# Optimization experiments

Measured on AMD Instinct MI355X. Metric: run time of the kernel, lower is better.

The kernel has to match this reference:

```python
import jax, jax.numpy as jnp
import numpy as np

NEG_SLOPE = 0.01  # torch nn.LeakyReLU default; module's alpha arg is unused in forward


def setup_inputs() -> dict:
    key = jax.random.key(0)
    k1, k2, k3, k4 = jax.random.split(key, 4)
    N, IN, OUT = 16384, 256, 128
    x = jax.random.normal(k1, (N, IN), dtype=jnp.float32)
    W_tran = jax.random.normal(k2, (OUT, IN), dtype=jnp.float32) / np.sqrt(IN)
    a1 = jax.random.normal(k3, (OUT,), dtype=jnp.float32) / np.sqrt(OUT)
    a2 = jax.random.normal(k4, (OUT,), dtype=jnp.float32) / np.sqrt(OUT)
    return {"x": x, "W_tran": W_tran, "a1": a1, "a2": a2}


def reference(x, W_tran, a1, a2):
    # h = tran(x): [N, out]
    h = x @ W_tran.T
    # att1(h) -> [N], att2(h) -> [N]
    s1 = h @ a1
    s2 = h @ a2
    # e[i, j] = leakyrelu(s2[i] + s1[j])  (unsqueeze(0) broadcasts att1 over rows)
    e = jax.nn.leaky_relu(s2[:, None] + s1[None, :], negative_slope=NEG_SLOPE)  # [N, N]
    return e @ h  # [N, out]
```

## Files before the change

### kernel.cpp

```cpp
#include <hip/hip_runtime.h>
#include <hip/hip_bf16.h>
#include <stdint.h>

#define NR 16384
#define KI 256
#define MO 128
#define ALPHA 0.01f
#define CH 32
#define NCH (NR / CH)
#define RB 4
#define JT 256
#define NJ (NR / JT)

typedef unsigned long long u64;
typedef __attribute__((ext_vector_type(8))) short bf16x8;
typedef __attribute__((ext_vector_type(4))) float f32x4;

static __device__ __forceinline__ unsigned xf(float f) {
    unsigned u = __float_as_uint(f);
    return u ^ (((unsigned)((int)u >> 31)) | 0x80000000u);
}

static __device__ __forceinline__ ushort2 cvt2(float a, float b) {
    __hip_bfloat162 r = __float22bfloat162_rn(make_float2(a, b));
    return *reinterpret_cast<ushort2*>(&r);
}

static __device__ __forceinline__ unsigned f2b(float f) {
    unsigned x = __float_as_uint(f);
    return (x + 0x7fffu + ((x >> 16) & 1u)) >> 16;
}
static __device__ __forceinline__ float b2f(unsigned u) {
    return __uint_as_float(u << 16);
}
static __device__ __forceinline__ unsigned pk(float hv, float sv) {
    return f2b(hv) | (f2b(sv) << 16);
}

__global__ __launch_bounds__(256) void k_gemm_fused(const float* __restrict__ x,
                                                    const float* __restrict__ w,
                                                    const float* __restrict__ a1,
                                                    const float* __restrict__ a2,
                                                    ushort* __restrict__ hb,
                                                    float* __restrict__ s1,
                                                    float* __restrict__ s2,
                                                    unsigned* __restrict__ keys,
                                                    int* __restrict__ rank) {
    __shared__ ushort Abf[64][40];
    __shared__ ushort Bbf[128][40];
    const int t = threadIdx.x;
    const int lane = t & 63;
    const int wv = t >> 6;
    const int rowBase = blockIdx.x * 64;
    const int xr = t >> 2, xc = (t & 3) << 3;
    const int wr = t >> 1, wc = (t & 1) << 4;
    const int fr = lane & 15;
    const int fk = (lane >> 4) << 3;

    f32x4 acc[8] = {};

    float4 xv0 = *(const float4*)&x[(size_t)(rowBase + xr) * KI + xc];
    float4 xv1 = *(const float4*)&x[(size_t)(rowBase + xr) * KI + xc + 4];
    float4 wv0 = *(const float4*)&w[(size_t)wr * KI + wc];
    float4 wv1 = *(const float4*)&w[(size_t)wr * KI + wc + 4];
    float4 wv2 = *(const float4*)&w[(size_t)wr * KI + wc + 8];
    float4 wv3 = *(const float4*)&w[(size_t)wr * KI + wc + 12];

    for (int ks = 0; ks < KI / 32; ++ks) {
        __syncthreads();
        {
            union { ushort2 u2[4]; bf16x8 v; } ap;
            ap.u2[0] = cvt2(xv0.x, xv0.y); ap.u2[1] = cvt2(xv0.z, xv0.w);
            ap.u2[2] = cvt2(xv1.x, xv1.y); ap.u2[3] = cvt2(xv1.z, xv1.w);
            *(bf16x8*)&Abf[xr][xc] = ap.v;
            union { ushort2 u2[4]; bf16x8 v; } bp0, bp1;
            bp0.u2[0] = cvt2(wv0.x, wv0.y); bp0.u2[1] = cvt2(wv0.z, wv0.w);
            bp0.u2[2] = cvt2(wv1.x, wv1.y); bp0.u2[3] = cvt2(wv1.z, wv1.w);
            bp1.u2[0] = cvt2(wv2.x, wv2.y); bp1.u2[1] = cvt2(wv2.z, wv2.w);
            bp1.u2[2] = cvt2(wv3.x, wv3.y); bp1.u2[3] = cvt2(wv3.z, wv3.w);
            *(bf16x8*)&Bbf[wr][wc] = bp0.v;
            *(bf16x8*)&Bbf[wr][wc + 8] = bp1.v;
        }
        __syncthreads();
        if (ks + 1 < KI / 32) {
            int k0 = (ks + 1) * 32;
            xv0 = *(const float4*)&x[(size_t)(rowBase + xr) * KI + k0 + xc];
            xv1 = *(const float4*)&x[(size_t)(rowBase + xr) * KI + k0 + xc + 4];
            wv0 = *(const float4*)&w[(size_t)wr * KI + k0 + wc];
            wv1 = *(const float4*)&w[(size_t)wr * KI + k0 + wc + 4];
            wv2 = *(const float4*)&w[(size_t)wr * KI + k0 + wc + 8];
            wv3 = *(const float4*)&w[(size_t)wr * KI + k0 + wc + 12];
        }
        bf16x8 af = *(const bf16x8*)&Abf[wv * 16 + fr][fk];
#pragma unroll
        for (int n = 0; n < 8; ++n) {
            bf16x8 bfr = *(const bf16x8*)&Bbf[n * 16 + fr][fk];
            acc[n] = __builtin_amdgcn_mfma_f32_16x16x32_bf16(af, bfr, acc[n], 0, 0, 0);
        }
    }

    const int rq = lane >> 4;
#pragma unroll
    for (int n = 0; n < 8; ++n)
#pragma unroll
        for (int r = 0; r < 4; ++r)
            hb[(size_t)(rowBase + wv * 16 + rq * 4 + r) * MO + n * 16 + fr] = (ushort)f2b(acc[n][r]);

    float a1v[8], a2v[8];
#pragma unroll
    for (int n = 0; n < 8; ++n) { a1v[n] = a1[n * 16 + fr]; a2v[n] = a2[n * 16 + fr]; }
#pragma unroll
    for (int r = 0; r < 4; ++r) {
        float p1 = 0.f, p2 = 0.f;
#pragma unroll
        for (int n = 0; n < 8; ++n) {
            p1 = fmaf(acc[n][r], a1v[n], p1);
            p2 = fmaf(acc[n][r], a2v[n], p2);
        }
#pragma unroll
        for (int off = 8; off; off >>= 1) {
            p1 += __shfl_xor(p1, off, 64);
            p2 += __shfl_xor(p2, off, 64);
        }
        if (fr == 0) {
            int row = rowBase + wv * 16 + rq * 4 + r;
            s1[row] = p1;
            s2[row] = p2;
            keys[row] = (xf(p1) & 0xFFFFC000u) | (unsigned)row;
            rank[row] = 0;
        }
    }
}

__global__ __launch_bounds__(256) void k_rank(const unsigned* __restrict__ keys,
                                              int* __restrict__ rank) {
    __shared__ unsigned sk[JT];
    const int t = threadIdx.x;
    const int ibase = blockIdx.x * (256 * RB);
    const int jbase = blockIdx.y * JT;
    sk[t] = keys[jbase + t];
    unsigned ki[RB];
#pragma unroll
    for (int k = 0; k < RB; ++k) ki[k] = keys[ibase + k * 256 + t];
    int cnt[RB] = {};
    __syncthreads();
#pragma unroll 4
    for (int jj = 0; jj < JT; ++jj) {
        unsigned kj = sk[jj];
#pragma unroll
        for (int k = 0; k < RB; ++k)
            cnt[k] += (kj < ki[k]) ? 1 : 0;
    }
#pragma unroll
    for (int k = 0; k < RB; ++k)
        atomicAdd(&rank[ibase + k * 256 + t], cnt[k]);
}

__global__ __launch_bounds__(256) void k_scatter(const float* __restrict__ s1,
                                                 const int* __restrict__ rank,
                                                 float* __restrict__ s1s,
                                                 int* __restrict__ perm) {
    int i = blockIdx.x * 256 + threadIdx.x;
    int r = rank[i];
    s1s[r] = s1[i];
    perm[r] = i;
}

__global__ __launch_bounds__(256) void k_chunk(const ushort* __restrict__ hb,
                                               const int* __restrict__ perm,
                                               const float* __restrict__ s1s,
                                               const float* __restrict__ s2,
                                               unsigned* __restrict__ SHS,
                                               int* __restrict__ kidx) {
    __shared__ int pi[CH];
    __shared__ float ss[CH];
    __shared__ float rH[128], rS[128];
    const int t = threadIdx.x, c = t & 127, g = t >> 7, q = blockIdx.x;
    if (t < CH) { pi[t] = perm[q * CH + t]; ss[t] = s1s[q * CH + t]; }
    __syncthreads();
    float v[16];
#pragma unroll
    for (int m = 0; m < 16; ++m)
        v[m] = b2f(hb[(size_t)pi[g * 16 + m] * MO + c]);
    if (g == 1) {
        float runH = 0.f, runS = 0.f;
#pragma unroll
        for (int m = 15; m >= 0; --m) {
            runH += v[m];
            runS = fmaf(ss[16 + m], v[m], runS);
            SHS[(size_t)(q * CH + 16 + m) * MO + c] = pk(runH, runS);
        }
        rH[c] = runH; rS[c] = runS;
    } else if (t < CH) {
        int i = q * CH + t;
        unsigned qtv = xf(-s2[i]) & 0xFFFFC000u;
        int lo = 0, hi = NR;
        while (lo < hi) {
            int mid = (lo + hi) >> 1;
            if ((xf(s1s[mid]) & 0xFFFFC000u) < qtv) lo = mid + 1; else hi = mid;
        }
        kidx[i] = lo;
    }
    __syncthreads();
    if (g == 0) {
        float runH = rH[c], runS = rS[c];
#pragma unroll
        for (int m = 15; m >= 0; --m) {
            runH += v[m];
            runS = fmaf(ss[m], v[m], runS);
            SHS[(size_t)(q * CH + m) * MO + c] = pk(runH, runS);
        }
    }
    if (q == NCH - 1 && t < 128) SHS[(size_t)NR * MO + t] = 0u;
}

__global__ __launch_bounds__(512) void k_scan(const unsigned* __restrict__ SHS,
                                              float2* __restrict__ cSuf) {
    __shared__ float bufH[NCH], bufS[NCH];
    const int c = blockIdx.x, q = threadIdx.x;
    unsigned hu = SHS[(size_t)(q * CH) * MO + c];
    float vh = b2f(hu & 0xffffu), vs = b2f(hu >> 16);
    bufH[q] = vh; bufS[q] = vs;
    __syncthreads();
#pragma unroll
    for (int off = 1; off < NCH; off <<= 1) {
        float ah = 0.f, as = 0.f;
        if (q + off < NCH) { ah = bufH[q + off]; as = bufS[q + off]; }
        __syncthreads();
        bufH[q] += ah; bufS[q] += as;
        __syncthreads();
    }
    cSuf[q * MO + c] = make_float2(bufH[q] - vh, bufS[q] - vs);
    if (q == 0) cSuf[(size_t)NCH * MO + c] = make_float2(0.f, 0.f);
}

__global__ __launch_bounds__(256) void k_final(const unsigned* __restrict__ SHS,
                                               const float2* __restrict__ cSuf,
                                               const float* __restrict__ s2,
                                               const int* __restrict__ kidx,
                                               float* __restrict__ out) {
    int idx = blockIdx.x * 256 + threadIdx.x;
    int i = idx >> 7, c = idx & 127;
    float s2v = s2[i];
    int k = kidx[i];
    unsigned w0u = SHS[c];
    float2 c0 = cSuf[c];
    unsigned wku = SHS[(size_t)k * MO + c];
    float2 ck = cSuf[(size_t)(k >> 5) * MO + c];
    float th  = b2f(w0u & 0xffffu) + c0.x, tsh  = b2f(w0u >> 16) + c0.y;
    float sh  = b2f(wku & 0xffffu) + ck.x, sshv = b2f(wku >> 16) + ck.y;
    out[idx] = ALPHA * fmaf(s2v, th, tsh) + (1.f - ALPHA) * fmaf(s2v, sh, sshv);
}

extern "C" void kernel_launch(void* const* d_in, const int* in_sizes, int n_in,
                              void* d_out, int out_size, void* d_ws, size_t ws_size,
                              hipStream_t stream) {
    const float* x  = (const float*)d_in[0];
    const float* w  = (const float*)d_in[1];
    const float* a1 = (const float*)d_in[2];
    const float* a2 = (const float*)d_in[3];
    float* out = (float*)d_out;

    char* ws = (char*)d_ws;
    ushort*   hb   = (ushort*)ws;
    unsigned* SHS  = (unsigned*)(ws + (size_t)NR * MO * 2);
    float2*   cSuf = (float2*)((char*)SHS + (size_t)(NR + 1) * MO * 4);
    float*    s1   = (float*)((char*)cSuf + (size_t)(NCH + 1) * MO * 8);
    float*    s2   = s1 + NR;
    float*    s1s  = s2 + NR;
    unsigned* keys = (unsigned*)(s1s + NR);
    int*      perm = (int*)(keys + NR);
    int*      kidx = perm + NR;
    int*      rank = kidx + NR;

    k_gemm_fused<<<NR / 64, 256, 0, stream>>>(x, w, a1, a2, hb, s1, s2, keys, rank);
    k_rank<<<dim3(NR / (256 * RB), NJ), 256, 0, stream>>>(keys, rank);
    k_scatter<<<NR / 256, 256, 0, stream>>>(s1, rank, s1s, perm);
    k_chunk<<<NCH, 256, 0, stream>>>(hb, perm, s1s, s2, SHS, kidx);
    k_scan<<<MO, NCH, 0, stream>>>(SHS, cSuf);
    k_final<<<(NR * MO) / 256, 256, 0, stream>>>(SHS, cSuf, s2, kidx, out);
}
```

Before: 54.97 us.

## Replace brute-force rank counting with chunk bitonic sort plus binary search

The O(N^2) all-pairs comparison used to compute each key's rank is replaced. A new kernel bitonic-sorts 512-key chunks in shared memory, and the rank kernel then binary-searches each key within every sorted chunk and accumulates the positions with atomics. This cuts the comparison work from N per key to about log2(512) probes per chunk. The cost is an extra kernel launch, a barrier-heavy bitonic sort, and data-dependent shared-memory reads that may cause bank conflicts.

```diff
diff --git a/kernel.cpp b/kernel.cpp
--- a/kernel.cpp
+++ b/kernel.cpp
@@ -8,9 +8,9 @@
 #define ALPHA 0.01f
 #define CH 32
 #define NCH (NR / CH)
+#define CK 512
+#define NCK (NR / CK)
 #define RB 4
-#define JT 256
-#define NJ (NR / JT)
 
 typedef unsigned long long u64;
 typedef __attribute__((ext_vector_type(8))) short bf16x8;
@@ -132,28 +132,53 @@
     }
 }
 
+__global__ __launch_bounds__(256) void k_sort(const unsigned* __restrict__ keys,
+                                              unsigned* __restrict__ skeys) {
+    __shared__ unsigned sk[CK];
+    const int t = threadIdx.x;
+    const int base = blockIdx.x * CK;
+    sk[t] = keys[base + t];
+    sk[t + 256] = keys[base + 256 + t];
+    __syncthreads();
+    for (int k = 2; k <= CK; k <<= 1) {
+        for (int j = k >> 1; j > 0; j >>= 1) {
+            int i = ((t & ~(j - 1)) << 1) | (t & (j - 1));
+            int p = i | j;
+            bool up = ((i & k) == 0);
+            unsigned a = sk[i], b = sk[p];
+            if ((a > b) == up) { sk[i] = b; sk[p] = a; }
+            __syncthreads();
+        }
+    }
+    skeys[base + t] = sk[t];
+    skeys[base + 256 + t] = sk[t + 256];
+}
+
 __global__ __launch_bounds__(256) void k_rank(const unsigned* __restrict__ keys,
+                                              const unsigned* __restrict__ skeys,
                                               int* __restrict__ rank) {
-    __shared__ unsigned sk[JT];
+    __shared__ unsigned sc[CK];
     const int t = threadIdx.x;
     const int ibase = blockIdx.x * (256 * RB);
-    const int jbase = blockIdx.y * JT;
-    sk[t] = keys[jbase + t];
+    const int cbase = blockIdx.y * CK;
+    sc[t] = skeys[cbase + t];
+    sc[t + 256] = skeys[cbase + 256 + t];
     unsigned ki[RB];
 #pragma unroll
     for (int k = 0; k < RB; ++k) ki[k] = keys[ibase + k * 256 + t];
-    int cnt[RB] = {};
-    __syncthreads();
-#pragma unroll 4
-    for (int jj = 0; jj < JT; ++jj) {
-        unsigned kj = sk[jj];
-#pragma unroll
-        for (int k = 0; k < RB; ++k)
-            cnt[k] += (kj < ki[k]) ? 1 : 0;
+    int pos[RB] = {};
+    __syncthreads();
+#pragma unroll
+    for (int step = CK; step; step >>= 1) {
+#pragma unroll
+        for (int k = 0; k < RB; ++k) {
+            int np = pos[k] + step;
+            if (np <= CK && sc[np - 1] < ki[k]) pos[k] = np;
+        }
     }
 #pragma unroll
     for (int k = 0; k < RB; ++k)
-        atomicAdd(&rank[ibase + k * 256 + t], cnt[k]);
+        atomicAdd(&rank[ibase + k * 256 + t], pos[k]);
 }
 
 __global__ __launch_bounds__(256) void k_scatter(const float* __restrict__ s1,
@@ -262,19 +287,21 @@
     float* out = (float*)d_out;
 
     char* ws = (char*)d_ws;
-    ushort*   hb   = (ushort*)ws;
-    unsigned* SHS  = (unsigned*)(ws + (size_t)NR * MO * 2);
-    float2*   cSuf = (float2*)((char*)SHS + (size_t)(NR + 1) * MO * 4);
-    float*    s1   = (float*)((char*)cSuf + (size_t)(NCH + 1) * MO * 8);
-    float*    s2   = s1 + NR;
-    float*    s1s  = s2 + NR;
-    unsigned* keys = (unsigned*)(s1s + NR);
-    int*      perm = (int*)(keys + NR);
-    int*      kidx = perm + NR;
-    int*      rank = kidx + NR;
+    ushort*   hb    = (ushort*)ws;
+    unsigned* SHS   = (unsigned*)(ws + (size_t)NR * MO * 2);
+    float2*   cSuf  = (float2*)((char*)SHS + (size_t)(NR + 1) * MO * 4);
+    float*    s1    = (float*)((char*)cSuf + (size_t)(NCH + 1) * MO * 8);
+    float*    s2    = s1 + NR;
+    float*    s1s   = s2 + NR;
+    unsigned* keys  = (unsigned*)(s1s + NR);
+    unsigned* skeys = keys + NR;
+    int*      perm  = (int*)(skeys + NR);
+    int*      kidx  = perm + NR;
+    int*      rank  = kidx + NR;
 
     k_gemm_fused<<<NR / 64, 256, 0, stream>>>(x, w, a1, a2, hb, s1, s2, keys, rank);
-    k_rank<<<dim3(NR / (256 * RB), NJ), 256, 0, stream>>>(keys, rank);
+    k_sort<<<NCK, 256, 0, stream>>>(keys, skeys);
+    k_rank<<<dim3(NR / (256 * RB), NCK), 256, 0, stream>>>(keys, skeys, rank);
     k_scatter<<<NR / 256, 256, 0, stream>>>(s1, rank, s1s, perm);
     k_chunk<<<NCH, 256, 0, stream>>>(hb, perm, s1s, s2, SHS, kidx);
     k_scan<<<MO, NCH, 0, stream>>>(SHS, cSuf);
```

Measured after the change: 47.36 us. 13.8% less time.

## Replace brute-force rank counting with per-chunk bitonic sort and binary search

Applied to the files above, without the earlier changes.

The rank kernel previously compared every key against every other key, which is O(N^2) comparisons. Now each block loads a 512-key chunk into shared memory, bitonic-sorts it, and finds each query key's count of smaller keys in that chunk by binary search. The grid shrinks to 32 chunks along y. In exchange, every block re-sorts its chunk, and the sort needs many __syncthreads steps.

```diff
diff --git a/kernel.cpp b/kernel.cpp
--- a/kernel.cpp
+++ b/kernel.cpp
@@ -8,9 +8,9 @@
 #define ALPHA 0.01f
 #define CH 32
 #define NCH (NR / CH)
+#define CK 512
+#define NCK (NR / CK)
 #define RB 4
-#define JT 256
-#define NJ (NR / JT)
 
 typedef unsigned long long u64;
 typedef __attribute__((ext_vector_type(8))) short bf16x8;
@@ -134,26 +134,38 @@
 
 __global__ __launch_bounds__(256) void k_rank(const unsigned* __restrict__ keys,
                                               int* __restrict__ rank) {
-    __shared__ unsigned sk[JT];
+    __shared__ unsigned sc[CK];
     const int t = threadIdx.x;
     const int ibase = blockIdx.x * (256 * RB);
-    const int jbase = blockIdx.y * JT;
-    sk[t] = keys[jbase + t];
+    const int cbase = blockIdx.y * CK;
+    sc[t] = keys[cbase + t];
+    sc[t + 256] = keys[cbase + 256 + t];
     unsigned ki[RB];
 #pragma unroll
     for (int k = 0; k < RB; ++k) ki[k] = keys[ibase + k * 256 + t];
-    int cnt[RB] = {};
-    __syncthreads();
-#pragma unroll 4
-    for (int jj = 0; jj < JT; ++jj) {
-        unsigned kj = sk[jj];
-#pragma unroll
-        for (int k = 0; k < RB; ++k)
-            cnt[k] += (kj < ki[k]) ? 1 : 0;
+    __syncthreads();
+    for (int k2 = 2; k2 <= CK; k2 <<= 1) {
+        for (int j = k2 >> 1; j > 0; j >>= 1) {
+            int i = ((t & ~(j - 1)) << 1) | (t & (j - 1));
+            int p = i | j;
+            bool up = ((i & k2) == 0);
+            unsigned a = sc[i], b = sc[p];
+            if ((a > b) == up) { sc[i] = b; sc[p] = a; }
+            __syncthreads();
+        }
+    }
+    int pos[RB] = {};
+#pragma unroll
+    for (int step = CK; step; step >>= 1) {
+#pragma unroll
+        for (int k = 0; k < RB; ++k) {
+            int np = pos[k] + step;
+            if (np <= CK && sc[np - 1] < ki[k]) pos[k] = np;
+        }
     }
 #pragma unroll
     for (int k = 0; k < RB; ++k)
-        atomicAdd(&rank[ibase + k * 256 + t], cnt[k]);
+        atomicAdd(&rank[ibase + k * 256 + t], pos[k]);
 }
 
 __global__ __launch_bounds__(256) void k_scatter(const float* __restrict__ s1,
@@ -274,7 +286,7 @@
     int*      rank = kidx + NR;
 
     k_gemm_fused<<<NR / 64, 256, 0, stream>>>(x, w, a1, a2, hb, s1, s2, keys, rank);
-    k_rank<<<dim3(NR / (256 * RB), NJ), 256, 0, stream>>>(keys, rank);
+    k_rank<<<dim3(NR / (256 * RB), NCK), 256, 0, stream>>>(keys, rank);
     k_scatter<<<NR / 256, 256, 0, stream>>>(s1, rank, s1s, perm);
     k_chunk<<<NCH, 256, 0, stream>>>(hb, perm, s1s, s2, SHS, kidx);
     k_scan<<<MO, NCH, 0, stream>>>(SHS, cSuf);
```

New measurement: 45.30 us, median of 2. 1.21x faster.
